# Kernel tuning notes

Measured on AMD Instinct MI355X. Metric: run time of the kernel, lower is better.

The kernel has to match this reference:

```python
import jax, jax.numpy as jnp
import numpy as np

B, S, D, H = 2, 2048, 2048, 16  # batch, seq, d_model, n_heads
LN_EPS = 1e-6  # flax nn.LayerNorm default


def _layernorm(x, scale):
    mu = jnp.mean(x, axis=-1, keepdims=True)
    var = jnp.var(x, axis=-1, keepdims=True)
    return (x - mu) * jax.lax.rsqrt(var + LN_EPS) * scale


def setup_inputs() -> dict:
    key = jax.random.key(0)
    ks = jax.random.split(key, 5)
    x = jax.random.normal(ks[0], (B, S, D), dtype=jnp.float32)
    # ALiBi-style bias, broadcastable over batch and query positions
    attn_bias = jax.random.normal(ks[1], (1, H, 1, S), dtype=jnp.float32)
    attention_mask = jnp.ones((B, S), dtype=jnp.int32)
    w_qkv = jax.random.normal(ks[2], (D, 3 * D), dtype=jnp.float32) * 0.01
    b_qkv = jnp.zeros((3 * D,), dtype=jnp.float32)
    wo = jax.random.normal(ks[3], (D, D), dtype=jnp.float32) * 0.01
    b_wo = jnp.zeros((D,), dtype=jnp.float32)
    q_ln_scale = jnp.ones((D,), dtype=jnp.float32)
    k_ln_scale = jnp.ones((D,), dtype=jnp.float32)
    return {"x": x, "attn_bias": attn_bias, "attention_mask": attention_mask,
            "w_qkv": w_qkv, "b_qkv": b_qkv, "wo": wo, "b_wo": b_wo,
            "q_ln_scale": q_ln_scale, "k_ln_scale": k_ln_scale}


def reference(x, attn_bias, attention_mask, w_qkv, b_qkv, wo, b_wo, q_ln_scale, k_ln_scale):
    b, s, ds = x.shape
    h = H
    d = ds // h  # head dim
    qkv = jnp.einsum('bsd,df->bsf', x, w_qkv) + b_qkv
    q, k, v = jnp.split(qkv, 3, axis=-1)
    # qk-LayerNorm is over the FULL d_model, before head split (as in source)
    q = _layernorm(q, q_ln_scale)
    k = _layernorm(k, k_ln_scale)
    q = q.reshape(b, s, h, d)
    k = k.reshape(b, s, h, d)
    v = v.reshape(b, s, h, d)
    atw = jnp.einsum('bqhd,bkhd->bhqk', q, k) * jax.lax.rsqrt(jnp.asarray(d, v.dtype))
    atw = atw + attn_bias  # ALiBi bias
    mv = jnp.finfo(atw.dtype).min
    # causal mask [1,1,s,s]
    causal = jnp.tril(jnp.ones((s, s), dtype=bool))[None, None]
    # padding mask: 0 where attended, min where masked
    pad = jnp.where(attention_mask.reshape(b, 1, 1, s) == 1, 0.0, mv).astype(atw.dtype)
    atw = atw + pad
    atw = atw + jnp.where(causal, 0.0, mv).astype(atw.dtype)
    atw = jax.nn.softmax(atw, axis=-1)
    out = jnp.einsum('bhqk,bkhd->bqhd', atw, v).reshape(b, s, ds)
    return jnp.einsum('bsd,de->bse', out, wo) + b_wo
```

## Files before the change

kernel.cpp:

```cpp
#include <hip/hip_runtime.h>
#include <stdint.h>
#include <stddef.h>


typedef __attribute__((ext_vector_type(8))) short bf16x8;
typedef __attribute__((ext_vector_type(4))) float f32x4;

#define MFMA16(a, b, c) __builtin_amdgcn_mfma_f32_16x16x32_bf16((a), (b), (c), 0, 0, 0)

__device__ __forceinline__ void async_copy16(void* lds, const void* g) {
  __builtin_amdgcn_global_load_lds(
      (const __attribute__((address_space(1))) void*)g,
      (__attribute__((address_space(3))) void*)lds, 16, 0, 0);
}

__device__ __forceinline__ short f2bf(float f) {
  union { float f; uint32_t u; } v; v.f = f;
  uint32_t r = (v.u + 0x7fffu + ((v.u >> 16) & 1u)) >> 16;
  return (short)(uint16_t)r;
}

__global__ __launch_bounds__(256) void cvt_f32_bf16(const float* __restrict__ in,
                                                    short* __restrict__ out) {
  size_t i = ((size_t)blockIdx.x * 256 + threadIdx.x) * 8;
  f32x4 a = *(const f32x4*)(in + i);
  f32x4 b = *(const f32x4*)(in + i + 4);
  bf16x8 o;
#pragma unroll
  for (int j = 0; j < 4; ++j) { o[j] = f2bf(a[j]); o[4 + j] = f2bf(b[j]); }
  *(bf16x8*)(out + i) = o;
}

__global__ __launch_bounds__(256) void transpose_cvt(const float* __restrict__ in,
                                                     short* __restrict__ out,
                                                     int R, int C) {
  __shared__ float t[64][65];
  const int tid = threadIdx.x;
  const int c0 = blockIdx.x * 64, r0 = blockIdx.y * 64;
#pragma unroll
  for (int i = 0; i < 16; ++i) {
    int idx = i * 256 + tid;
    int r = idx >> 6, c = idx & 63;
    t[r][c] = in[(size_t)(r0 + r) * C + c0 + c];
  }
  __syncthreads();
#pragma unroll
  for (int i = 0; i < 16; ++i) {
    int idx = i * 256 + tid;
    int cc = idx >> 6, rr = idx & 63;
    out[(size_t)(c0 + cc) * R + r0 + rr] = f2bf(t[rr][cc]);
  }
}

__global__ __launch_bounds__(256) void transpose_v(const float* __restrict__ qkv,
                                                   short* __restrict__ vt) {
  __shared__ float t[64][65];
  const int tid = threadIdx.x;
  const int d0 = blockIdx.x * 64;
  const int s0 = blockIdx.y * 64;
  const int bh = blockIdx.z;
  const int b = bh >> 4, h = bh & 15;
#pragma unroll
  for (int i = 0; i < 16; ++i) {
    int idx = i * 256 + tid;
    int r = idx >> 6, c = idx & 63;
    t[r][c] = qkv[(size_t)(b * 2048 + s0 + r) * 6144 + 4096 + h * 128 + d0 + c];
  }
  __syncthreads();
#pragma unroll
  for (int i = 0; i < 16; ++i) {
    int idx = i * 256 + tid;
    int dd = idx >> 6, ss = idx & 63;
    vt[((size_t)(bh * 128 + d0 + dd)) * 2048 + s0 + ss] = f2bf(t[ss][dd]);
  }
}

__global__ __launch_bounds__(256) void ln_qk(const float* __restrict__ qkv,
                                             const float* __restrict__ qsc,
                                             const float* __restrict__ ksc,
                                             short* __restrict__ q_bf,
                                             short* __restrict__ k_bf) {
  __shared__ float redS[2][4], redQ[2][4];
  const int row = blockIdx.x, tid = threadIdx.x;
  const int lane = tid & 63, wave = tid >> 6;
  const float* base = qkv + (size_t)row * 6144;
#pragma unroll
  for (int part = 0; part < 2; ++part) {
    const float* p = base + part * 2048 + tid * 8;
    f32x4 va = *(const f32x4*)p;
    f32x4 vb = *(const f32x4*)(p + 4);
    float s = 0.f, sq = 0.f;
#pragma unroll
    for (int j = 0; j < 4; ++j) {
      s += va[j] + vb[j];
      sq += va[j] * va[j] + vb[j] * vb[j];
    }
#pragma unroll
    for (int d = 1; d < 64; d <<= 1) { s += __shfl_xor(s, d); sq += __shfl_xor(sq, d); }
    if (lane == 0) { redS[part][wave] = s; redQ[part][wave] = sq; }
    __syncthreads();
    float tot  = redS[part][0] + redS[part][1] + redS[part][2] + redS[part][3];
    float totq = redQ[part][0] + redQ[part][1] + redQ[part][2] + redQ[part][3];
    float mean = tot * (1.f / 2048.f);
    float var  = totq * (1.f / 2048.f) - mean * mean;
    float rstd = rsqrtf(var + 1e-6f);
    const float* scp = (part == 0 ? qsc : ksc) + tid * 8;
    f32x4 s0 = *(const f32x4*)scp;
    f32x4 s1 = *(const f32x4*)(scp + 4);
    bf16x8 o;
#pragma unroll
    for (int j = 0; j < 4; ++j) {
      o[j]     = f2bf((va[j] - mean) * rstd * s0[j]);
      o[4 + j] = f2bf((vb[j] - mean) * rstd * s1[j]);
    }
    short* outp = (part == 0 ? q_bf : k_bf) + (size_t)row * 2048 + tid * 8;
    *(bf16x8*)outp = o;
  }
}

__global__ __launch_bounds__(256, 2) void gemm_bt_bias(const short* __restrict__ A,
                                                       const short* __restrict__ BT,
                                                       const float* __restrict__ bias,
                                                       float* __restrict__ C,
                                                       int M, int N, int K) {
  __shared__ alignas(16) short a_lds[128 * 32];
  __shared__ alignas(16) short b_lds[128 * 32];
  const int tid = threadIdx.x;
  const int lane = tid & 63, wave = tid >> 6;
  const int wr = wave >> 1, wc = wave & 1;
  const int tn = blockIdx.x, tm = blockIdx.y;
  const int r15 = lane & 15, hi = lane >> 4;

  const short* Ab = A + (size_t)tm * 128 * K;
  const short* Bb = BT + (size_t)tn * 128 * K;

  f32x4 acc[4][4];
  const f32x4 Z = {0.f, 0.f, 0.f, 0.f};
#pragma unroll
  for (int m = 0; m < 4; ++m)
#pragma unroll
    for (int n = 0; n < 4; ++n) acc[m][n] = Z;

  for (int k0 = 0; k0 < K; k0 += 32) {
    __syncthreads();
#pragma unroll
    for (int j = 0; j < 2; ++j) {
      int c = j * 256 + tid;
      int row = c >> 2, col = (c & 3) << 3;
      async_copy16(&a_lds[c << 3], Ab + (size_t)row * K + k0 + col);
      async_copy16(&b_lds[c << 3], Bb + (size_t)row * K + k0 + col);
    }
    __syncthreads();
    bf16x8 af[4], bfr[4];
#pragma unroll
    for (int m = 0; m < 4; ++m)
      af[m] = *(const bf16x8*)&a_lds[(wr * 64 + m * 16 + r15) * 32 + hi * 8];
#pragma unroll
    for (int n = 0; n < 4; ++n)
      bfr[n] = *(const bf16x8*)&b_lds[(wc * 64 + n * 16 + r15) * 32 + hi * 8];
#pragma unroll
    for (int m = 0; m < 4; ++m)
#pragma unroll
      for (int n = 0; n < 4; ++n) acc[m][n] = MFMA16(af[m], bfr[n], acc[m][n]);
  }

  const int r0 = tm * 128 + wr * 64;
  const int c0 = tn * 128 + wc * 64;
#pragma unroll
  for (int n = 0; n < 4; ++n) {
    float bv = bias[c0 + n * 16 + r15];
#pragma unroll
    for (int m = 0; m < 4; ++m) {
#pragma unroll
      for (int r = 0; r < 4; ++r) {
        C[(size_t)(r0 + m * 16 + hi * 4 + r) * N + c0 + n * 16 + r15] =
            acc[m][n][r] + bv;
      }
    }
  }
}

#define ATT_SCALE 0.08838834764831845f

__global__ __launch_bounds__(256) void attn_fwd(const short* __restrict__ q_bf,
                                                const short* __restrict__ k_bf,
                                                const short* __restrict__ vt,
                                                const float* __restrict__ abias,
                                                const int* __restrict__ amask,
                                                short* __restrict__ out_bf) {
  __shared__ alignas(16) short K_lds[64 * 128];
  __shared__ alignas(16) short V_lds[128 * 64];
  __shared__ alignas(16) short p_lds[4][16 * 64];
  __shared__ float bias_c[2048];

  const int tid = threadIdx.x, lane = tid & 63, wave = tid >> 6;
  const int qt = 31 - blockIdx.x;
  const int h = blockIdx.y, b = blockIdx.z;
  const int r15 = lane & 15, hi = lane >> 4;

  for (int i = tid; i < 2048; i += 256) {
    float bb = abias[h * 2048 + i];
    if (amask[b * 2048 + i] == 0) bb = -1e30f;
    bias_c[i] = bb;
  }

  const int qrow = b * 2048 + qt * 64 + wave * 16 + r15;
  bf16x8 qf[4];
#pragma unroll
  for (int kb = 0; kb < 4; ++kb)
    qf[kb] = *(const bf16x8*)(q_bf + (size_t)qrow * 2048 + h * 128 + kb * 32 + hi * 8);

  f32x4 O[8];
  const f32x4 Z = {0.f, 0.f, 0.f, 0.f};
#pragma unroll
  for (int n = 0; n < 8; ++n) O[n] = Z;
  float m_run[4], l_run[4];
#pragma unroll
  for (int r = 0; r < 4; ++r) { m_run[r] = -3e38f; l_run[r] = 0.f; }

  __syncthreads();

  const int ntiles = qt + 1;
  for (int kt = 0; kt < ntiles; ++kt) {
#pragma unroll
    for (int j = 0; j < 4; ++j) {
      int c = j * 256 + tid;
      int kr = c >> 4, kc = (c & 15) ^ (kr & 7);
      async_copy16(&K_lds[c << 3],
                   k_bf + (size_t)(b * 2048 + kt * 64 + kr) * 2048 + h * 128 + (kc << 3));
      int vr = c >> 3, vc = (c & 7) ^ (vr & 7);
      async_copy16(&V_lds[c << 3],
                   vt + ((size_t)((b * 16 + h) * 128 + vr)) * 2048 + kt * 64 + (vc << 3));
    }
    __syncthreads();

    f32x4 s[4];
#pragma unroll
    for (int ks = 0; ks < 4; ++ks) {
      s[ks] = Z;
#pragma unroll
      for (int kb = 0; kb < 4; ++kb) {
        int row = ks * 16 + r15;
        int ch = (kb * 4 + hi) ^ (row & 7);
        bf16x8 kf = *(const bf16x8*)&K_lds[row * 128 + ch * 8];
        s[ks] = MFMA16(qf[kb], kf, s[ks]);
      }
    }

    const bool diag = (kt == qt);
    const int qg0 = qt * 64 + wave * 16 + hi * 4;
#pragma unroll
    for (int ks = 0; ks < 4; ++ks) {
      int kg = kt * 64 + ks * 16 + r15;
      float bb = bias_c[kg];
#pragma unroll
      for (int r = 0; r < 4; ++r) {
        float v = s[ks][r] * ATT_SCALE + bb;
        if (diag && (kg > qg0 + r)) v = -1e30f;
        s[ks][r] = v;
      }
    }

    float corr[4];
#pragma unroll
    for (int r = 0; r < 4; ++r) {
      float mx = fmaxf(fmaxf(s[0][r], s[1][r]), fmaxf(s[2][r], s[3][r]));
      mx = fmaxf(mx, __shfl_xor(mx, 1));
      mx = fmaxf(mx, __shfl_xor(mx, 2));
      mx = fmaxf(mx, __shfl_xor(mx, 4));
      mx = fmaxf(mx, __shfl_xor(mx, 8));
      float mn = fmaxf(m_run[r], mx);
      corr[r] = __expf(m_run[r] - mn);
      m_run[r] = mn;
      float sum = 0.f;
#pragma unroll
      for (int ks = 0; ks < 4; ++ks) {
        float p = __expf(s[ks][r] - mn);
        s[ks][r] = p;
        sum += p;
      }
      sum += __shfl_xor(sum, 1);
      sum += __shfl_xor(sum, 2);
      sum += __shfl_xor(sum, 4);
      sum += __shfl_xor(sum, 8);
      l_run[r] = l_run[r] * corr[r] + sum;
    }

#pragma unroll
    for (int n = 0; n < 8; ++n)
#pragma unroll
      for (int r = 0; r < 4; ++r) O[n][r] *= corr[r];

    short* pw = &p_lds[wave][0];
#pragma unroll
    for (int ks = 0; ks < 4; ++ks)
#pragma unroll
      for (int r = 0; r < 4; ++r) {
        int q = hi * 4 + r;
        int k = ks * 16 + r15;
        pw[q * 64 + (k ^ ((q & 7) << 3))] = f2bf(s[ks][r]);
      }

    bf16x8 pf[2];
#pragma unroll
    for (int kb = 0; kb < 2; ++kb)
      pf[kb] = *(const bf16x8*)&pw[r15 * 64 + ((kb * 32 + hi * 8) ^ ((r15 & 7) << 3))];

#pragma unroll
    for (int n = 0; n < 8; ++n) {
#pragma unroll
      for (int kb = 0; kb < 2; ++kb) {
        int row = n * 16 + r15;
        int ch = (kb * 4 + hi) ^ (row & 7);
        bf16x8 vf = *(const bf16x8*)&V_lds[row * 64 + ch * 8];
        O[n] = MFMA16(pf[kb], vf, O[n]);
      }
    }
    __syncthreads();
  }

  float inv[4];
#pragma unroll
  for (int r = 0; r < 4; ++r) inv[r] = 1.0f / l_run[r];
  const int orow = b * 2048 + qt * 64 + wave * 16;
#pragma unroll
  for (int n = 0; n < 8; ++n)
#pragma unroll
    for (int r = 0; r < 4; ++r)
      out_bf[(size_t)(orow + hi * 4 + r) * 2048 + h * 128 + n * 16 + r15] =
          f2bf(O[n][r] * inv[r]);
}

extern "C" void kernel_launch(void* const* d_in, const int* in_sizes, int n_in,
                              void* d_out, int out_size, void* d_ws, size_t ws_size,
                              hipStream_t stream) {
  const float* x     = (const float*)d_in[0];
  const float* abias = (const float*)d_in[1];
  const int*   amask = (const int*)d_in[2];
  const float* w_qkv = (const float*)d_in[3];
  const float* b_qkv = (const float*)d_in[4];
  const float* wo    = (const float*)d_in[5];
  const float* b_wo  = (const float*)d_in[6];
  const float* q_ln  = (const float*)d_in[7];
  const float* k_ln  = (const float*)d_in[8];
  float* out = (float*)d_out;

  char* ws = (char*)d_ws;
  short* x_bf   = (short*)(ws);
  short* wqkvT  = (short*)(ws + 16777216);
  short* woT    = (short*)(ws + 41943040);
  short* q_bf   = (short*)(ws + 50331648);
  short* k_bf   = (short*)(ws + 67108864);
  short* vt     = (short*)(ws + 83886080);
  short* out_bf = (short*)(ws + 100663296);
  float* qkv    = (float*)(ws + 117440512);

  cvt_f32_bf16<<<4096, 256, 0, stream>>>(x, x_bf);
  transpose_cvt<<<dim3(96, 32), 256, 0, stream>>>(w_qkv, wqkvT, 2048, 6144);
  transpose_cvt<<<dim3(32, 32), 256, 0, stream>>>(wo, woT, 2048, 2048);
  gemm_bt_bias<<<dim3(48, 32), 256, 0, stream>>>(x_bf, wqkvT, b_qkv, qkv,
                                                 4096, 6144, 2048);
  ln_qk<<<4096, 256, 0, stream>>>(qkv, q_ln, k_ln, q_bf, k_bf);
  transpose_v<<<dim3(2, 32, 32), 256, 0, stream>>>(qkv, vt);
  attn_fwd<<<dim3(32, 16, 2), 256, 0, stream>>>(q_bf, k_bf, vt, abias, amask, out_bf);
  gemm_bt_bias<<<dim3(16, 32), 256, 0, stream>>>(out_bf, woT, b_wo, out,
                                                 4096, 2048, 2048);
}
```

Measured before the change: 411.7 us.

## Store QKV intermediate in bf16 and streamline attention softmax bookkeeping

The QKV projection GEMM now writes bf16 instead of fp32, and the LayerNorm and V-transpose kernels read bf16. This halves intermediate memory traffic at the cost of rounding pre-LayerNorm activations to bf16. The attention kernel also changes in several ways: the softmax scale is folded into Q during LayerNorm, the causal-mask branch runs only on diagonal tiles, packed bf16 conversion is used for P, and the row sum is computed with an extra MFMA against a ones vector instead of shuffles. The barrier placement is also moved, with an explicit vmcnt drain after the async loads.

```diff
diff --git a/kernel.cpp b/kernel.cpp
--- a/kernel.cpp
+++ b/kernel.cpp
@@ -19,6 +19,15 @@
   uint32_t r = (v.u + 0x7fffu + ((v.u >> 16) & 1u)) >> 16;
   return (short)(uint16_t)r;
 }
+
+__device__ __forceinline__ float bf2f(short s) {
+  union { float f; uint32_t u; } v;
+  v.u = ((uint32_t)(uint16_t)s) << 16;
+  return v.f;
+}
+
+#define ATT_SCALE 0.08838834764831845f
+#define VMDRAIN asm volatile("s_waitcnt vmcnt(0)" ::: "memory")
 
 __global__ __launch_bounds__(256) void cvt_f32_bf16(const float* __restrict__ in,
                                                     short* __restrict__ out) {
@@ -52,9 +61,9 @@
   }
 }
 
-__global__ __launch_bounds__(256) void transpose_v(const float* __restrict__ qkv,
-                                                   short* __restrict__ vt) {
-  __shared__ float t[64][65];
+__global__ __launch_bounds__(256) void transpose_v_bf(const short* __restrict__ qkv,
+                                                      short* __restrict__ vt) {
+  __shared__ short t[64][65];
   const int tid = threadIdx.x;
   const int d0 = blockIdx.x * 64;
   const int s0 = blockIdx.y * 64;
@@ -71,11 +80,11 @@
   for (int i = 0; i < 16; ++i) {
     int idx = i * 256 + tid;
     int dd = idx >> 6, ss = idx & 63;
-    vt[((size_t)(bh * 128 + d0 + dd)) * 2048 + s0 + ss] = f2bf(t[ss][dd]);
-  }
-}
-
-__global__ __launch_bounds__(256) void ln_qk(const float* __restrict__ qkv,
+    vt[((size_t)(bh * 128 + d0 + dd)) * 2048 + s0 + ss] = t[ss][dd];
+  }
+}
+
+__global__ __launch_bounds__(256) void ln_qk(const short* __restrict__ qkv,
                                              const float* __restrict__ qsc,
                                              const float* __restrict__ ksc,
                                              short* __restrict__ q_bf,
@@ -83,18 +92,17 @@
   __shared__ float redS[2][4], redQ[2][4];
   const int row = blockIdx.x, tid = threadIdx.x;
   const int lane = tid & 63, wave = tid >> 6;
-  const float* base = qkv + (size_t)row * 6144;
+  const short* base = qkv + (size_t)row * 6144;
 #pragma unroll
   for (int part = 0; part < 2; ++part) {
-    const float* p = base + part * 2048 + tid * 8;
-    f32x4 va = *(const f32x4*)p;
-    f32x4 vb = *(const f32x4*)(p + 4);
+    const short* p = base + part * 2048 + tid * 8;
+    bf16x8 v8 = *(const bf16x8*)p;
+    float f[8];
+#pragma unroll
+    for (int j = 0; j < 8; ++j) f[j] = bf2f(v8[j]);
     float s = 0.f, sq = 0.f;
 #pragma unroll
-    for (int j = 0; j < 4; ++j) {
-      s += va[j] + vb[j];
-      sq += va[j] * va[j] + vb[j] * vb[j];
-    }
+    for (int j = 0; j < 8; ++j) { s += f[j]; sq += f[j] * f[j]; }
 #pragma unroll
     for (int d = 1; d < 64; d <<= 1) { s += __shfl_xor(s, d); sq += __shfl_xor(sq, d); }
     if (lane == 0) { redS[part][wave] = s; redQ[part][wave] = sq; }
@@ -103,25 +111,26 @@
     float totq = redQ[part][0] + redQ[part][1] + redQ[part][2] + redQ[part][3];
     float mean = tot * (1.f / 2048.f);
     float var  = totq * (1.f / 2048.f) - mean * mean;
-    float rstd = rsqrtf(var + 1e-6f);
+    float rstd = rsqrtf(var + 1e-6f) * (part == 0 ? ATT_SCALE : 1.0f);
     const float* scp = (part == 0 ? qsc : ksc) + tid * 8;
     f32x4 s0 = *(const f32x4*)scp;
     f32x4 s1 = *(const f32x4*)(scp + 4);
     bf16x8 o;
 #pragma unroll
     for (int j = 0; j < 4; ++j) {
-      o[j]     = f2bf((va[j] - mean) * rstd * s0[j]);
-      o[4 + j] = f2bf((vb[j] - mean) * rstd * s1[j]);
+      o[j]     = f2bf((f[j] - mean) * rstd * s0[j]);
+      o[4 + j] = f2bf((f[4 + j] - mean) * rstd * s1[j]);
     }
     short* outp = (part == 0 ? q_bf : k_bf) + (size_t)row * 2048 + tid * 8;
     *(bf16x8*)outp = o;
   }
 }
 
+template <typename OutT>
 __global__ __launch_bounds__(256, 2) void gemm_bt_bias(const short* __restrict__ A,
                                                        const short* __restrict__ BT,
                                                        const float* __restrict__ bias,
-                                                       float* __restrict__ C,
+                                                       OutT* __restrict__ C,
                                                        int M, int N, int K) {
   __shared__ alignas(16) short a_lds[128 * 32];
   __shared__ alignas(16) short b_lds[128 * 32];
@@ -173,14 +182,14 @@
     for (int m = 0; m < 4; ++m) {
 #pragma unroll
       for (int r = 0; r < 4; ++r) {
-        C[(size_t)(r0 + m * 16 + hi * 4 + r) * N + c0 + n * 16 + r15] =
-            acc[m][n][r] + bv;
-      }
-    }
-  }
-}
-
-#define ATT_SCALE 0.08838834764831845f
+        float val = acc[m][n][r] + bv;
+        size_t idx = (size_t)(r0 + m * 16 + hi * 4 + r) * N + c0 + n * 16 + r15;
+        if constexpr (sizeof(OutT) == 2) C[idx] = (OutT)f2bf(val);
+        else                             C[idx] = val;
+      }
+    }
+  }
+}
 
 __global__ __launch_bounds__(256) void attn_fwd(const short* __restrict__ q_bf,
                                                 const short* __restrict__ k_bf,
@@ -214,14 +223,20 @@
   const f32x4 Z = {0.f, 0.f, 0.f, 0.f};
 #pragma unroll
   for (int n = 0; n < 8; ++n) O[n] = Z;
-  float m_run[4], l_run[4];
-#pragma unroll
-  for (int r = 0; r < 4; ++r) { m_run[r] = -3e38f; l_run[r] = 0.f; }
-
-  __syncthreads();
-
+  f32x4 Ol = Z;
+  float m_run[4];
+#pragma unroll
+  for (int r = 0; r < 4; ++r) m_run[r] = -3e38f;
+
+  const short one_bf = (short)0x3F80;
+  const bf16x8 ones_f = {one_bf, one_bf, one_bf, one_bf,
+                         one_bf, one_bf, one_bf, one_bf};
+  const int qg0 = qt * 64 + wave * 16 + hi * 4;
   const int ntiles = qt + 1;
+
   for (int kt = 0; kt < ntiles; ++kt) {
+    __syncthreads();
+
 #pragma unroll
     for (int j = 0; j < 4; ++j) {
       int c = j * 256 + tid;
@@ -232,6 +247,7 @@
       async_copy16(&V_lds[c << 3],
                    vt + ((size_t)((b * 16 + h) * 128 + vr)) * 2048 + kt * 64 + (vc << 3));
     }
+    VMDRAIN;
     __syncthreads();
 
     f32x4 s[4];
@@ -247,17 +263,24 @@
       }
     }
 
-    const bool diag = (kt == qt);
-    const int qg0 = qt * 64 + wave * 16 + hi * 4;
-#pragma unroll
-    for (int ks = 0; ks < 4; ++ks) {
-      int kg = kt * 64 + ks * 16 + r15;
-      float bb = bias_c[kg];
-#pragma unroll
-      for (int r = 0; r < 4; ++r) {
-        float v = s[ks][r] * ATT_SCALE + bb;
-        if (diag && (kg > qg0 + r)) v = -1e30f;
-        s[ks][r] = v;
+    if (kt == qt) {
+#pragma unroll
+      for (int ks = 0; ks < 4; ++ks) {
+        int kg = kt * 64 + ks * 16 + r15;
+        float bb = bias_c[kg];
+#pragma unroll
+        for (int r = 0; r < 4; ++r) {
+          float v = s[ks][r] + bb;
+          if (kg > qg0 + r) v = -1e30f;
+          s[ks][r] = v;
+        }
+      }
+    } else {
+#pragma unroll
+      for (int ks = 0; ks < 4; ++ks) {
+        float bb = bias_c[kt * 64 + ks * 16 + r15];
+#pragma unroll
+        for (int r = 0; r < 4; ++r) s[ks][r] += bb;
       }
     }
 
@@ -272,34 +295,29 @@
       float mn = fmaxf(m_run[r], mx);
       corr[r] = __expf(m_run[r] - mn);
       m_run[r] = mn;
-      float sum = 0.f;
-#pragma unroll
-      for (int ks = 0; ks < 4; ++ks) {
-        float p = __expf(s[ks][r] - mn);
-        s[ks][r] = p;
-        sum += p;
-      }
-      sum += __shfl_xor(sum, 1);
-      sum += __shfl_xor(sum, 2);
-      sum += __shfl_xor(sum, 4);
-      sum += __shfl_xor(sum, 8);
-      l_run[r] = l_run[r] * corr[r] + sum;
-    }
-
-#pragma unroll
-    for (int n = 0; n < 8; ++n)
-#pragma unroll
-      for (int r = 0; r < 4; ++r) O[n][r] *= corr[r];
+#pragma unroll
+      for (int ks = 0; ks < 4; ++ks) s[ks][r] = __expf(s[ks][r] - mn);
+    }
+#pragma unroll
+    for (int r = 0; r < 4; ++r) {
+      Ol[r] *= corr[r];
+#pragma unroll
+      for (int n = 0; n < 8; ++n) O[n][r] *= corr[r];
+    }
 
     short* pw = &p_lds[wave][0];
 #pragma unroll
-    for (int ks = 0; ks < 4; ++ks)
-#pragma unroll
-      for (int r = 0; r < 4; ++r) {
-        int q = hi * 4 + r;
-        int k = ks * 16 + r15;
-        pw[q * 64 + (k ^ ((q & 7) << 3))] = f2bf(s[ks][r]);
-      }
+    for (int r = 0; r < 4; ++r) {
+      int q = hi * 4 + r;
+      int qs = (q & 7) << 3;
+      uint32_t pk0, pk1;
+      asm("v_cvt_pk_bf16_f32 %0, %1, %2" : "=v"(pk0) : "v"(s[0][r]), "v"(s[1][r]));
+      asm("v_cvt_pk_bf16_f32 %0, %1, %2" : "=v"(pk1) : "v"(s[2][r]), "v"(s[3][r]));
+      pw[q * 64 + ((r15) ^ qs)]      = (short)pk0;
+      pw[q * 64 + ((16 + r15) ^ qs)] = (short)(pk0 >> 16);
+      pw[q * 64 + ((32 + r15) ^ qs)] = (short)pk1;
+      pw[q * 64 + ((48 + r15) ^ qs)] = (short)(pk1 >> 16);
+    }
 
     bf16x8 pf[2];
 #pragma unroll
@@ -316,12 +334,13 @@
         O[n] = MFMA16(pf[kb], vf, O[n]);
       }
     }
-    __syncthreads();
+    Ol = MFMA16(pf[0], ones_f, Ol);
+    Ol = MFMA16(pf[1], ones_f, Ol);
   }
 
   float inv[4];
 #pragma unroll
-  for (int r = 0; r < 4; ++r) inv[r] = 1.0f / l_run[r];
+  for (int r = 0; r < 4; ++r) inv[r] = 1.0f / Ol[r];
   const int orow = b * 2048 + qt * 64 + wave * 16;
 #pragma unroll
   for (int n = 0; n < 8; ++n)
@@ -353,16 +372,16 @@
   short* k_bf   = (short*)(ws + 67108864);
   short* vt     = (short*)(ws + 83886080);
   short* out_bf = (short*)(ws + 100663296);
-  float* qkv    = (float*)(ws + 117440512);
+  short* qkv_bf = (short*)(ws + 117440512);
 
   cvt_f32_bf16<<<4096, 256, 0, stream>>>(x, x_bf);
   transpose_cvt<<<dim3(96, 32), 256, 0, stream>>>(w_qkv, wqkvT, 2048, 6144);
   transpose_cvt<<<dim3(32, 32), 256, 0, stream>>>(wo, woT, 2048, 2048);
-  gemm_bt_bias<<<dim3(48, 32), 256, 0, stream>>>(x_bf, wqkvT, b_qkv, qkv,
-                                                 4096, 6144, 2048);
-  ln_qk<<<4096, 256, 0, stream>>>(qkv, q_ln, k_ln, q_bf, k_bf);
-  transpose_v<<<dim3(2, 32, 32), 256, 0, stream>>>(qkv, vt);
+  gemm_bt_bias<short><<<dim3(48, 32), 256, 0, stream>>>(x_bf, wqkvT, b_qkv, qkv_bf,
+                                                        4096, 6144, 2048);
+  ln_qk<<<4096, 256, 0, stream>>>(qkv_bf, q_ln, k_ln, q_bf, k_bf);
+  transpose_v_bf<<<dim3(2, 32, 32), 256, 0, stream>>>(qkv_bf, vt);
   attn_fwd<<<dim3(32, 16, 2), 256, 0, stream>>>(q_bf, k_bf, vt, abias, amask, out_bf);
-  gemm_bt_bias<<<dim3(16, 32), 256, 0, stream>>>(out_bf, woT, b_wo, out,
-                                                 4096, 2048, 2048);
-}
+  gemm_bt_bias<float><<<dim3(16, 32), 256, 0, stream>>>(out_bf, woT, b_wo, out,
+                                                        4096, 2048, 2048);
+}
```

Measured after the change: 378.2 us (median of 2 runs). 1.09x faster.
